# Optimization experiments

Measured on AMD Instinct MI355X. Metric: run time of the kernel, lower is better.

The kernel has to match this reference:

```python
import jax, jax.numpy as jnp
import numpy as np

B, TT, C, H, S, DF = 4, 2048, 2048, 32, 64, 7168
TC = 512            # chunk_len
NC = TT // TC       # number of chunks
N_LAYER, LAYER_ID = 12, 1
EPS = 1e-5
HS_DIV = float(np.sqrt(S))  # head_size_divisor


def layernorm(x, g, b):
    m = jnp.mean(x, axis=-1, keepdims=True)
    v = jnp.mean(jnp.square(x - m), axis=-1, keepdims=True)
    return (x - m) * jax.lax.rsqrt(v + EPS) * g + b


def time_shift(x):  # ZeroPad2d((0,0,1,-1)): x[t] <- x[t-1], x[0] <- 0
    return jnp.pad(x, ((0, 0), (1, 0), (0, 0)))[:, :-1, :]


def setup_inputs() -> dict:
    key = jax.random.key(0)
    ks = jax.random.split(key, 8)
    r10 = 1.0 - LAYER_ID / N_LAYER          # ratio_1_to_almost0
    r01 = LAYER_ID / (N_LAYER - 1)          # ratio_0_to_1
    ddd = np.arange(C, dtype=np.float64) / C
    f32 = lambda a: jnp.asarray(a, jnp.float32)
    hh = np.arange(H, dtype=np.float64)
    scale = 0.02
    W = lambda k, sh: (jax.random.normal(k, sh, jnp.float32) * scale)
    return {
        'x': jax.random.normal(ks[0], (B, TT, C), jnp.float32),
        'ln1_g': jnp.ones((C,), jnp.float32), 'ln1_b': jnp.zeros((C,), jnp.float32),
        'ln2_g': jnp.ones((C,), jnp.float32), 'ln2_b': jnp.zeros((C,), jnp.float32),
        'att_mix_k': f32(ddd ** r10),
        'att_mix_v': f32(ddd ** r10 + 0.3 * r01),
        'att_mix_r': f32(ddd ** (0.5 * r10)),
        'time_decay': f32(-8.0 + 7.0 * (hh / (H - 1)) ** (0.7 + 1.3 * r01)),
        'time_faaaa': jnp.full((H,), 0.05, jnp.float32),
        'Wr': W(ks[1], (C, C)), 'Wk': W(ks[2], (C, C)),
        'Wv': W(ks[3], (C, C)), 'Wo': W(ks[4], (C, C)),
        'lnx_g': jnp.ones((C,), jnp.float32), 'lnx_b': jnp.zeros((C,), jnp.float32),
        'ffn_mix_k': f32(ddd ** r10), 'ffn_mix_r': f32(ddd ** r10),
        'Wfk': W(ks[5], (C, DF)), 'Wfr': W(ks[6], (C, C)), 'Wfv': W(ks[7], (DF, C)),
    }


def _forward(x, ln1_g, ln1_b, ln2_g, ln2_b, att_mix_k, att_mix_v, att_mix_r,
             time_decay, time_faaaa, Wr, Wk, Wv, Wo, lnx_g, lnx_b,
             ffn_mix_k, ffn_mix_r, Wfk, Wfr, Wfv):
    # ---- RWKV5 TimeMix on ln1(x) ----
    h1 = layernorm(x, ln1_g, ln1_b)
    xx = time_shift(h1)
    xk = h1 * att_mix_k + xx * (1.0 - att_mix_k)
    xv = h1 * att_mix_v + xx * (1.0 - att_mix_v)
    xr = h1 * att_mix_r + xx * (1.0 - att_mix_r)
    r = (xr @ Wr).reshape(B, TT, H, S).transpose(0, 2, 1, 3)  # [B,H,TT,S]
    k = (xk @ Wk).reshape(B, TT, H, S).transpose(0, 2, 1, 3)
    v = (xv @ Wv).reshape(B, TT, H, S).transpose(0, 2, 1, 3)

    w = jnp.exp(-jnp.exp(time_decay))     # [H], per-head decay in (0,1)
    u = time_faaaa                         # [H], diagonal 'bonus'
    ws = w ** TC                           # chunk-level state decay
    t = jnp.arange(TC)
    wk = w[:, None] ** (TC - 1 - t)[None, :]   # [H,TC]: w^(T-1-t)
    wb = w[:, None] ** t[None, :]              # [H,TC]: w^t
    ii, jj = t[:, None], t[None, :]
    expo = jnp.where(jj < ii, ii - jj - 1, 0)
    # Wm[h,i,j] = w^(i-j-1) if j<i ; u if j==i ; 0 if j>i
    Wm = jnp.where(jj < ii, w[:, None, None] ** expo[None], 0.0)
    Wm = Wm + jnp.eye(TC, dtype=x.dtype)[None] * u[:, None, None]  # [H,TC,TC]

    rc = r.reshape(B, H, NC, TC, S).transpose(2, 0, 1, 3, 4)  # [NC,B,H,TC,S]
    kc = k.reshape(B, H, NC, TC, S).transpose(2, 0, 1, 3, 4)
    vc = v.reshape(B, H, NC, TC, S).transpose(2, 0, 1, 3, 4)

    def step(s, inp):  # s: [B,H,S,S] carried state
        rr, kk, vv = inp
        a = jnp.einsum('bhts,bhus->bhtu', rr, kk) * Wm[None]        # masked decay attn
        out = jnp.einsum('bhtu,bhus->bhts', a, vv)
        out = out + jnp.einsum('bhts,bhsu->bhtu', rr, s) * wb[None, :, :, None]
        s_new = ws[None, :, None, None] * s + jnp.einsum(
            'bhts,bhtu->bhsu', kk * wk[None, :, :, None], vv)
        return s_new, out

    s0 = jnp.zeros((B, H, S, S), x.dtype)
    _, xout = jax.lax.scan(step, s0, (rc, kc, vc))  # [NC,B,H,TC,S]
    xa = xout.transpose(1, 0, 3, 2, 4).reshape(B, TT, H, S)

    # GroupNorm(H groups over C) on x / sqrt(head_size)
    xa = xa / HS_DIV
    m = jnp.mean(xa, axis=-1, keepdims=True)
    va = jnp.mean(jnp.square(xa - m), axis=-1, keepdims=True)
    xa = (xa - m) * jax.lax.rsqrt(va + EPS)
    xa = xa * lnx_g.reshape(H, S) + lnx_b.reshape(H, S)
    x = x + xa.reshape(B, TT, C) @ Wo

    # ---- ChannelMix (gated squared-ReLU FFN) on ln2(x) ----
    h2 = layernorm(x, ln2_g, ln2_b)
    xx2 = time_shift(h2)
    xk2 = h2 * ffn_mix_k + xx2 * (1.0 - ffn_mix_k)
    xr2 = h2 * ffn_mix_r + xx2 * (1.0 - ffn_mix_r)
    kf = jnp.square(jax.nn.relu(xk2 @ Wfk))
    kv = kf @ Wfv
    return x + jax.nn.sigmoid(xr2 @ Wfr) * kv


def reference(x, ln1_g, ln1_b, ln2_g, ln2_b, att_mix_k, att_mix_v, att_mix_r,
              time_decay, time_faaaa, Wr, Wk, Wv, Wo, lnx_g, lnx_b,
              ffn_mix_k, ffn_mix_r, Wfk, Wfr, Wfv):
    return _forward(x, ln1_g, ln1_b, ln2_g, ln2_b, att_mix_k, att_mix_v,
                    att_mix_r, time_decay, time_faaaa, Wr, Wk, Wv, Wo,
                    lnx_g, lnx_b, ffn_mix_k, ffn_mix_r, Wfk, Wfr, Wfv)
```

## Files before the change

### kernel.cpp

```cpp
#include <hip/hip_runtime.h>

#define B_   4
#define TT_  2048
#define C_   2048
#define H_   32
#define S_   64
#define DF_  7168
#define TCH  512
#define NCH  4

typedef unsigned short u16;
typedef __bf16 bf16x8 __attribute__((ext_vector_type(8)));
typedef float  f32x4  __attribute__((ext_vector_type(4)));

__device__ __forceinline__ u16 f2bf(float f) {
  unsigned u = __builtin_bit_cast(unsigned, f);
  u = u + 0x7FFFu + ((u >> 16) & 1u);
  return (u16)(u >> 16);
}
__device__ __forceinline__ float bf2f(u16 v) {
  unsigned u = ((unsigned)v) << 16;
  return __builtin_bit_cast(float, u);
}

#define GLOAD16(g, l) __builtin_amdgcn_global_load_lds( \
    (const __attribute__((address_space(1))) void*)(g), \
    (__attribute__((address_space(3))) void*)(l), 16, 0, 0)

__device__ __forceinline__ void vmcnt6() { asm volatile("s_waitcnt vmcnt(6)" ::: "memory"); }
__device__ __forceinline__ void vmcnt0() { asm volatile("s_waitcnt vmcnt(0)" ::: "memory"); }

__global__ __launch_bounds__(256) void wcvt_t(const float* __restrict__ W,
                                              u16* __restrict__ Wt, int K, int Nfull,
                                              int n0off) {
  __shared__ alignas(16) float tile[32][33];
  int nloc = blockIdx.x * 32, k0 = blockIdx.y * 32;
  int tx = threadIdx.x & 31, ty = threadIdx.x >> 5;
  for (int r = ty; r < 32; r += 8)
    tile[r][tx] = W[(size_t)(k0 + r) * Nfull + n0off + nloc + tx];
  __syncthreads();
  for (int r = ty; r < 32; r += 8)
    Wt[(size_t)(nloc + r) * K + k0 + tx] = f2bf(tile[tx][r]);
}

__global__ __launch_bounds__(256) void ln_rows(const float* __restrict__ x,
                                               const float* __restrict__ g,
                                               const float* __restrict__ b,
                                               u16* __restrict__ out) {
  const int row = blockIdx.x;
  const float* xr = x + (size_t)row * C_;
  float v[8]; float s = 0.f, s2 = 0.f;
#pragma unroll
  for (int i = 0; i < 8; i++) { v[i] = xr[threadIdx.x + i * 256]; s += v[i]; s2 += v[i] * v[i]; }
#pragma unroll
  for (int o = 32; o > 0; o >>= 1) { s += __shfl_down(s, o); s2 += __shfl_down(s2, o); }
  __shared__ float rs[4], rs2[4];
  int wid = threadIdx.x >> 6, lane = threadIdx.x & 63;
  if (lane == 0) { rs[wid] = s; rs2[wid] = s2; }
  __syncthreads();
  s = rs[0] + rs[1] + rs[2] + rs[3];
  s2 = rs2[0] + rs2[1] + rs2[2] + rs2[3];
  float m = s * (1.f / C_);
  float var = s2 * (1.f / C_) - m * m;
  float inv = rsqrtf(var + 1e-5f);
  u16* orow = out + (size_t)row * C_;
#pragma unroll
  for (int i = 0; i < 8; i++) {
    int c = threadIdx.x + i * 256;
    orow[c] = f2bf((v[i] - m) * inv * g[c] + b[c]);
  }
}

__global__ void wtabs_k(const float* __restrict__ td, float* __restrict__ wb_tab,
                        float* __restrict__ wk_tab, float* __restrict__ wspow) {
  int h = blockIdx.x, t = threadIdx.x;
  float w = expf(-expf(td[h]));
  wb_tab[h * TCH + t] = powf(w, (float)t);
  wk_tab[h * TCH + t] = powf(w, (float)(TCH - 1 - t));
  if (t == 0) wspow[h] = powf(w, (float)TCH);
}

__device__ __forceinline__ void mix_body(const u16* cur, const u16* prev, bool hasp,
                                         const float* mc, u16* dst) {
  ushort4 c0 = *(const ushort4*)cur;
  ushort4 c1 = *(const ushort4*)(cur + 4);
  ushort4 p0 = {0, 0, 0, 0}, p1 = {0, 0, 0, 0};
  if (hasp) { p0 = *(const ushort4*)prev; p1 = *(const ushort4*)(prev + 4); }
  float4 mA = *(const float4*)mc;
  float4 mB = *(const float4*)(mc + 4);
  ushort4 r0, r1;
  r0.x = f2bf(bf2f(c0.x) * mA.x + bf2f(p0.x) * (1.f - mA.x));
  r0.y = f2bf(bf2f(c0.y) * mA.y + bf2f(p0.y) * (1.f - mA.y));
  r0.z = f2bf(bf2f(c0.z) * mA.z + bf2f(p0.z) * (1.f - mA.z));
  r0.w = f2bf(bf2f(c0.w) * mA.w + bf2f(p0.w) * (1.f - mA.w));
  r1.x = f2bf(bf2f(c1.x) * mB.x + bf2f(p1.x) * (1.f - mB.x));
  r1.y = f2bf(bf2f(c1.y) * mB.y + bf2f(p1.y) * (1.f - mB.y));
  r1.z = f2bf(bf2f(c1.z) * mB.z + bf2f(p1.z) * (1.f - mB.z));
  r1.w = f2bf(bf2f(c1.w) * mB.w + bf2f(p1.w) * (1.f - mB.w));
  *(ushort4*)dst = r0;
  *(ushort4*)(dst + 4) = r1;
}

__global__ __launch_bounds__(256) void mix3(const u16* __restrict__ h,
                                            const float* __restrict__ mk,
                                            const float* __restrict__ mv,
                                            const float* __restrict__ mr,
                                            u16* __restrict__ xk, u16* __restrict__ xv,
                                            u16* __restrict__ xr) {
  size_t i8 = (size_t)blockIdx.x * 256 + threadIdx.x;
  size_t off = i8 * 8;
  int c0 = (int)(off & (C_ - 1));
  int row = (int)(i8 >> 8);
  bool hasp = (row & (TT_ - 1)) != 0;
  const u16* cur = h + off;
  const u16* prev = cur - C_;
  mix_body(cur, prev, hasp, mk + c0, xk + off);
  mix_body(cur, prev, hasp, mv + c0, xv + off);
  mix_body(cur, prev, hasp, mr + c0, xr + off);
}

__global__ __launch_bounds__(256) void mix2(const u16* __restrict__ h,
                                            const float* __restrict__ mk,
                                            const float* __restrict__ mr,
                                            u16* __restrict__ xk, u16* __restrict__ xr) {
  size_t i8 = (size_t)blockIdx.x * 256 + threadIdx.x;
  size_t off = i8 * 8;
  int c0 = (int)(off & (C_ - 1));
  int row = (int)(i8 >> 8);
  bool hasp = (row & (TT_ - 1)) != 0;
  const u16* cur = h + off;
  const u16* prev = cur - C_;
  mix_body(cur, prev, hasp, mk + c0, xk + off);
  mix_body(cur, prev, hasp, mr + c0, xr + off);
}

template <int EPI>
__global__ __launch_bounds__(512) void gemm3(const u16* __restrict__ A,
                                             const u16* __restrict__ Bt,
                                             void* __restrict__ Cv,
                                             const float* __restrict__ res,
                                             const u16* __restrict__ srp,
                                             int N, int K, int lda, int ldb, int gy) {
  __shared__ alignas(16) char smem[3 * 49152];
  const int nwg = gridDim.x, qq = nwg >> 3;
  const int wg = (int)(blockIdx.x & 7) * qq + (int)(blockIdx.x >> 3);
  const int bx = wg / gy, by = wg % gy;
  const int tid = threadIdx.x, w = tid >> 6, lane = tid & 63;
  const int fr = lane & 15, fq = lane >> 4;
  const int m0 = bx * 128, n0 = by * 256;
  const int wm = (w >> 2) * 64, wn = (w & 3) * 64;
  const int rowS = tid >> 3;
  const int colS = ((tid & 7) * 8) ^ ((rowS & 7) << 3);
  const u16* Ag = A + (size_t)(m0 + rowS) * lda + colS;
  const u16* Bg = Bt + (size_t)(n0 + rowS) * ldb + colS;
  const int NT = K >> 6;

  f32x4 acc[4][4];
#pragma unroll
  for (int m = 0; m < 4; m++)
#pragma unroll
    for (int n = 0; n < 4; n++) acc[m][n] = (f32x4){0.f, 0.f, 0.f, 0.f};

#define STG_A(buf, k0, j) GLOAD16(Ag + (size_t)((j) * 64) * lda + (k0), \
    smem + (buf) * 49152 + (j) * 8192 + w * 1024)
#define STG_B(buf, k0, j) GLOAD16(Bg + (size_t)((j) * 64) * ldb + (k0), \
    smem + (buf) * 49152 + 16384 + (j) * 8192 + w * 1024)
#define RD_A(buf, kk, m) (*(const bf16x8*)(smem + (buf) * 49152 + \
    ((((wm + (m) * 16 + fr) * 128) + (kk) * 64 + fq * 16) ^ (((wm + (m) * 16 + fr) & 7) << 4))))
#define RD_B(buf, kk, n) (*(const bf16x8*)(smem + (buf) * 49152 + 16384 + \
    ((((wn + (n) * 16 + fr) * 128) + (kk) * 64 + fq * 16) ^ (((wn + (n) * 16 + fr) & 7) << 4))))

  STG_A(0, 0, 0); STG_A(0, 0, 1);
  STG_B(0, 0, 0); STG_B(0, 0, 1); STG_B(0, 0, 2); STG_B(0, 0, 3);
  STG_A(1, 64, 0); STG_A(1, 64, 1);
  STG_B(1, 64, 0); STG_B(1, 64, 1); STG_B(1, 64, 2); STG_B(1, 64, 3);
  vmcnt6();
  __builtin_amdgcn_s_barrier();

  int bufc = 0;
  for (int t = 0; t < NT; t++) {
    int b2 = bufc + 2; if (b2 >= 3) b2 -= 3;
    const bool st = (t + 2) < NT;
    const int k2 = (t + 2) << 6;
    bf16x8 av[4], bv[4];

#pragma unroll
    for (int m = 0; m < 4; m++) av[m] = RD_A(bufc, 0, m);
    bv[0] = RD_B(bufc, 0, 0); bv[1] = RD_B(bufc, 0, 1);
    if (st) STG_A(b2, k2, 0);
    __builtin_amdgcn_s_barrier();
    __builtin_amdgcn_s_setprio(1);
#pragma unroll
    for (int m = 0; m < 4; m++) {
      acc[m][0] = __builtin_amdgcn_mfma_f32_16x16x32_bf16(av[m], bv[0], acc[m][0], 0, 0, 0);
      acc[m][1] = __builtin_amdgcn_mfma_f32_16x16x32_bf16(av[m], bv[1], acc[m][1], 0, 0, 0);
    }
    __builtin_amdgcn_s_setprio(0);
    __builtin_amdgcn_s_barrier();

    bv[2] = RD_B(bufc, 0, 2); bv[3] = RD_B(bufc, 0, 3);
    if (st) { STG_A(b2, k2, 1); STG_B(b2, k2, 0); }
    __builtin_amdgcn_s_barrier();
    __builtin_amdgcn_s_setprio(1);
#pragma unroll
    for (int m = 0; m < 4; m++) {
      acc[m][2] = __builtin_amdgcn_mfma_f32_16x16x32_bf16(av[m], bv[2], acc[m][2], 0, 0, 0);
      acc[m][3] = __builtin_amdgcn_mfma_f32_16x16x32_bf16(av[m], bv[3], acc[m][3], 0, 0, 0);
    }
    __builtin_amdgcn_s_setprio(0);
    __builtin_amdgcn_s_barrier();

#pragma unroll
    for (int m = 0; m < 4; m++) av[m] = RD_A(bufc, 1, m);
    bv[0] = RD_B(bufc, 1, 0); bv[1] = RD_B(bufc, 1, 1);
    if (st) { STG_B(b2, k2, 1); STG_B(b2, k2, 2); }
    __builtin_amdgcn_s_barrier();
    __builtin_amdgcn_s_setprio(1);
#pragma unroll
    for (int m = 0; m < 4; m++) {
      acc[m][0] = __builtin_amdgcn_mfma_f32_16x16x32_bf16(av[m], bv[0], acc[m][0], 0, 0, 0);
      acc[m][1] = __builtin_amdgcn_mfma_f32_16x16x32_bf16(av[m], bv[1], acc[m][1], 0, 0, 0);
    }
    __builtin_amdgcn_s_setprio(0);
    __builtin_amdgcn_s_barrier();

    bv[2] = RD_B(bufc, 1, 2); bv[3] = RD_B(bufc, 1, 3);
    if (st) STG_B(b2, k2, 3);
    if (st) vmcnt6(); else vmcnt0();
    __builtin_amdgcn_s_barrier();
    __builtin_amdgcn_s_setprio(1);
#pragma unroll
    for (int m = 0; m < 4; m++) {
      acc[m][2] = __builtin_amdgcn_mfma_f32_16x16x32_bf16(av[m], bv[2], acc[m][2], 0, 0, 0);
      acc[m][3] = __builtin_amdgcn_mfma_f32_16x16x32_bf16(av[m], bv[3], acc[m][3], 0, 0, 0);
    }
    __builtin_amdgcn_s_setprio(0);
    __builtin_amdgcn_s_barrier();

    bufc = bufc + 1 == 3 ? 0 : bufc + 1;
  }
#undef STG_A
#undef STG_B
#undef RD_A
#undef RD_B

#pragma unroll
  for (int m = 0; m < 4; m++)
#pragma unroll
    for (int n = 0; n < 4; n++)
#pragma unroll
      for (int j = 0; j < 4; j++) {
        int row = m0 + wm + m * 16 + fq * 4 + j;
        int col = n0 + wn + n * 16 + fr;
        size_t idx = (size_t)row * N + col;
        float v = acc[m][n][j];
        if (EPI == 0) ((u16*)Cv)[idx] = f2bf(v);
        else if (EPI == 1) ((float*)Cv)[idx] = v + res[idx];
        else if (EPI == 2) { float r = v > 0.f ? v : 0.f; ((u16*)Cv)[idx] = f2bf(r * r); }
        else if (EPI == 3) ((u16*)Cv)[idx] = f2bf(1.f / (1.f + expf(-v)));
        else {
          float pvv = ((float*)Cv)[idx];
          ((float*)Cv)[idx] = pvv + bf2f(srp[idx]) * v;
        }
      }
}

__global__ __launch_bounds__(256) void kvsum_m(const u16* __restrict__ K,
                                               const u16* __restrict__ V,
                                               const float* __restrict__ wk_tab,
                                               float* __restrict__ SC) {
  const int bh = blockIdx.x & 127, c = blockIdx.x >> 7;
  const int b = bh >> 5, h = bh & 31;
  const int tid = threadIdx.x, w = tid >> 6, lane = tid & 63;
  const int fr = lane & 15, fq = lane >> 4;
  const size_t chunkbase = (size_t)b * TT_ + (size_t)c * TCH;
  const u16* Kp = K + chunkbase * C_ + h * 64;
  const u16* Vp = V + chunkbase * C_ + h * 64;
  __shared__ alignas(16) u16 Kts[64 * 128];
  __shared__ alignas(16) u16 Vts[64 * 128];
  f32x4 acc[4];
#pragma unroll
  for (int n = 0; n < 4; n++) acc[n] = (f32x4){0.f, 0.f, 0.f, 0.f};

  for (int tb = 0; tb < 4; tb++) {
    __syncthreads();
    const int u = tid >> 1;
    const int tg = tb * 128 + u;
    const float wkv = wk_tab[h * TCH + tg];
#pragma unroll
    for (int i = 0; i < 4; i++) {
      int s0 = (tid & 1) * 32 + i * 8;
      uint4 dK = *(const uint4*)(Kp + (size_t)tg * C_ + s0);
      uint4 dV = *(const uint4*)(Vp + (size_t)tg * C_ + s0);
      const u16* ek = (const u16*)&dK;
      const u16* ev = (const u16*)&dV;
#pragma unroll
      for (int j = 0; j < 8; j++) {
        int s = s0 + j;
        int byte = s * 256 + u * 2;
        byte ^= (s & 7) << 4;
        *(u16*)((char*)Kts + byte) = f2bf(bf2f(ek[j]) * wkv);
        *(u16*)((char*)Vts + byte) = ev[j];
      }
    }
    __syncthreads();
#pragma unroll
    for (int kk = 0; kk < 4; kk++) {
      int rbyteA = (w * 16 + fr) * 256 + kk * 64 + fq * 16;
      rbyteA ^= (fr & 7) << 4;
      bf16x8 av = *(const bf16x8*)((char*)Kts + rbyteA);
#pragma unroll
      for (int n = 0; n < 4; n++) {
        int rbyteB = (n * 16 + fr) * 256 + kk * 64 + fq * 16;
        rbyteB ^= (fr & 7) << 4;
        bf16x8 bv = *(const bf16x8*)((char*)Vts + rbyteB);
        acc[n] = __builtin_amdgcn_mfma_f32_16x16x32_bf16(av, bv, acc[n], 0, 0, 0);
      }
    }
  }
  float* out = SC + ((size_t)c * 128 + bh) * 4096;
#pragma unroll
  for (int n = 0; n < 4; n++)
#pragma unroll
    for (int j = 0; j < 4; j++) {
      int srow = w * 16 + fq * 4 + j;
      int scol = n * 16 + fr;
      out[srow * 64 + scol] = acc[n][j];
    }
}

__global__ __launch_bounds__(256) void stcomb(const float* __restrict__ SC,
                                              u16* __restrict__ STt,
                                              const float* __restrict__ wspow) {
  const int bh = blockIdx.x;
  const float ws = wspow[bh & 31];
  const int tid = threadIdx.x;
#pragma unroll
  for (int e = 0; e < 16; e++) {
    int idxT = e * 256 + tid;
    int s = idxT >> 6, sp = idxT & 63;
    int src = sp * 64 + s;
    float st = 0.f;
#pragma unroll
    for (int c = 0; c < 4; c++) {
      STt[((size_t)c * 128 + bh) * 4096 + idxT] = f2bf(st);
      st = ws * st + SC[((size_t)c * 128 + bh) * 4096 + src];
    }
  }
}

__global__ __launch_bounds__(256) void att_out_m(const u16* __restrict__ R,
                                                 const u16* __restrict__ K,
                                                 const u16* __restrict__ V,
                                                 const u16* __restrict__ STt,
                                                 const float* __restrict__ wb_tab,
                                                 const float* __restrict__ u_vec,
                                                 u16* __restrict__ xa) {
  const int bh = blockIdx.x;
  const int ti = blockIdx.y;
  const int c  = blockIdx.z;
  const int b = bh >> 5, h = bh & 31;
  const int tid = threadIdx.x, w = tid >> 6, lane = tid & 63;
  const int fr = lane & 15, fq = lane >> 4;
  const int t0 = ti * 64;
  const size_t chunkbase = (size_t)b * TT_ + (size_t)c * TCH;
  const u16* Rp = R + (chunkbase + t0) * C_ + h * 64;
  const u16* Kp = K + chunkbase * C_ + h * 64;
  const u16* Vp = V + chunkbase * C_ + h * 64;

  __shared__ alignas(16) u16 Rs[64 * 64];
  __shared__ alignas(16) u16 Ks[64 * 64];
  __shared__ alignas(16) u16 Vts[64 * 64];
  __shared__ alignas(16) u16 Xs[64 * 64];
  __shared__ float wbs[512];

#pragma unroll
  for (int it = 0; it < 2; it++) {
    int r = (tid >> 3) + it * 32;
    int cb = (tid & 7) * 16;
    uint4 d = *(const uint4*)((const char*)(Rp + (size_t)r * C_) + cb);
    int byte = (r * 128 + cb) ^ ((r & 7) << 4);
    *(uint4*)((char*)Rs + byte) = d;
  }
  const u16* stg = STt + ((size_t)c * 128 + bh) * 4096;
#pragma unroll
  for (int it = 0; it < 2; it++) {
    int s = (tid >> 3) + it * 32;
    int cb = (tid & 7) * 16;
    uint4 d = *(const uint4*)((const char*)(stg + (size_t)s * 64) + cb);
    int byte = (s * 128 + cb) ^ ((s & 7) << 4);
    *(uint4*)((char*)Xs + byte) = d;
  }
  wbs[tid] = wb_tab[h * TCH + tid];
  wbs[tid + 256] = wb_tab[h * TCH + tid + 256];
  const float uh = u_vec[h];
  __syncthreads();

  f32x4 pv[4];
#pragma unroll
  for (int n = 0; n < 4; n++) pv[n] = (f32x4){0.f, 0.f, 0.f, 0.f};
#pragma unroll
  for (int kk = 0; kk < 2; kk++) {
    int rbA = ((w * 16 + fr) * 128 + kk * 64 + fq * 16) ^ ((fr & 7) << 4);
    bf16x8 av = *(const bf16x8*)((char*)Rs + rbA);
#pragma unroll
    for (int n = 0; n < 4; n++) {
      int rbB = ((n * 16 + fr) * 128 + kk * 64 + fq * 16) ^ ((fr & 7) << 4);
      bf16x8 bv = *(const bf16x8*)((char*)Xs + rbB);
      pv[n] = __builtin_amdgcn_mfma_f32_16x16x32_bf16(av, bv, pv[n], 0, 0, 0);
    }
  }
#pragma unroll
  for (int n = 0; n < 4; n++)
#pragma unroll
    for (int j = 0; j < 4; j++) {
      int tg = t0 + w * 16 + fq * 4 + j;
      pv[n][j] *= wbs[tg];
    }

  for (int ub = 0; ub <= ti; ub++) {
    const int u0 = ub * 64;
    __syncthreads();
#pragma unroll
    for (int it = 0; it < 2; it++) {
      int r = (tid >> 3) + it * 32;
      int cb = (tid & 7) * 16;
      uint4 d = *(const uint4*)((const char*)(Kp + (size_t)(u0 + r) * C_) + cb);
      int byte = (r * 128 + cb) ^ ((r & 7) << 4);
      *(uint4*)((char*)Ks + byte) = d;
    }
#pragma unroll
    for (int it = 0; it < 2; it++) {
      int u = (tid >> 3) + it * 32;
      int s0 = (tid & 7) * 8;
      uint4 d = *(const uint4*)(Vp + (size_t)(u0 + u) * C_ + s0);
      const u16* ev = (const u16*)&d;
#pragma unroll
      for (int j = 0; j < 8; j++) {
        int s = s0 + j;
        int byte = (s * 128 + u * 2) ^ ((s & 7) << 4);
        *(u16*)((char*)Vts + byte) = ev[j];
      }
    }
    __syncthreads();
    f32x4 accA[4];
#pragma unroll
    for (int n = 0; n < 4; n++) accA[n] = (f32x4){0.f, 0.f, 0.f, 0.f};
#pragma unroll
    for (int kk = 0; kk < 2; kk++) {
      int rbA = ((w * 16 + fr) * 128 + kk * 64 + fq * 16) ^ ((fr & 7) << 4);
      bf16x8 av = *(const bf16x8*)((char*)Rs + rbA);
#pragma unroll
      for (int n = 0; n < 4; n++) {
        int rbB = ((n * 16 + fr) * 128 + kk * 64 + fq * 16) ^ ((fr & 7) << 4);
        bf16x8 bv = *(const bf16x8*)((char*)Ks + rbB);
        accA[n] = __builtin_amdgcn_mfma_f32_16x16x32_bf16(av, bv, accA[n], 0, 0, 0);
      }
    }
#pragma unroll
    for (int n = 0; n < 4; n++) {
#pragma unroll
      for (int j = 0; j < 4; j++) {
        int tl = w * 16 + fq * 4 + j;
        int tg = t0 + tl;
        int u = u0 + n * 16 + fr;
        int d = tg - u;
        float f = (d > 0) ? wbs[d - 1] : ((d == 0) ? uh : 0.f);
        int byte = (tl * 128 + (n * 16 + fr) * 2) ^ ((tl & 7) << 4);
        *(u16*)((char*)Xs + byte) = f2bf(accA[n][j] * f);
      }
    }
#pragma unroll
    for (int kk = 0; kk < 2; kk++) {
      int rbA = ((w * 16 + fr) * 128 + kk * 64 + fq * 16) ^ ((fr & 7) << 4);
      bf16x8 ap = *(const bf16x8*)((char*)Xs + rbA);
#pragma unroll
      for (int n = 0; n < 4; n++) {
        int rbB = ((n * 16 + fr) * 128 + kk * 64 + fq * 16) ^ ((fr & 7) << 4);
        bf16x8 vp = *(const bf16x8*)((char*)Vts + rbB);
        pv[n] = __builtin_amdgcn_mfma_f32_16x16x32_bf16(ap, vp, pv[n], 0, 0, 0);
      }
    }
  }
  u16* xout = xa + (chunkbase + t0) * C_ + h * 64;
#pragma unroll
  for (int n = 0; n < 4; n++)
#pragma unroll
    for (int j = 0; j < 4; j++) {
      int tl = w * 16 + fq * 4 + j;
      xout[(size_t)tl * C_ + n * 16 + fr] = f2bf(pv[n][j]);
    }
}

__global__ __launch_bounds__(256) void gnorm(const u16* __restrict__ xa,
                                             const float* __restrict__ g,
                                             const float* __restrict__ b,
                                             u16* __restrict__ out) {
  const int row = blockIdx.x;
  const int lane = threadIdx.x & 63, wv = threadIdx.x >> 6;
  const u16* xp = xa + (size_t)row * C_;
  u16* op = out + (size_t)row * C_;
  for (int h = wv; h < 32; h += 4) {
    float v = bf2f(xp[h * 64 + lane]) * 0.125f;
    float s = v, s2 = v * v;
#pragma unroll
    for (int o = 32; o > 0; o >>= 1) { s += __shfl_down(s, o); s2 += __shfl_down(s2, o); }
    s = __shfl(s, 0); s2 = __shfl(s2, 0);
    float m = s * (1.f / 64.f), var = s2 * (1.f / 64.f) - m * m;
    float nv = (v - m) * rsqrtf(var + 1e-5f);
    op[h * 64 + lane] = f2bf(nv * g[h * 64 + lane] + b[h * 64 + lane]);
  }
}

extern "C" void kernel_launch(void* const* d_in, const int* in_sizes, int n_in,
                              void* d_out, int out_size, void* d_ws, size_t ws_size,
                              hipStream_t stream) {
  (void)in_sizes; (void)n_in; (void)out_size; (void)ws_size;
  const float* x    = (const float*)d_in[0];
  const float* ln1g = (const float*)d_in[1];
  const float* ln1b = (const float*)d_in[2];
  const float* ln2g = (const float*)d_in[3];
  const float* ln2b = (const float*)d_in[4];
  const float* amk  = (const float*)d_in[5];
  const float* amv  = (const float*)d_in[6];
  const float* amr  = (const float*)d_in[7];
  const float* tdec = (const float*)d_in[8];
  const float* tfaa = (const float*)d_in[9];
  const float* Wr   = (const float*)d_in[10];
  const float* Wk   = (const float*)d_in[11];
  const float* Wv   = (const float*)d_in[12];
  const float* Wo   = (const float*)d_in[13];
  const float* lnxg = (const float*)d_in[14];
  const float* lnxb = (const float*)d_in[15];
  const float* fmk  = (const float*)d_in[16];
  const float* fmr  = (const float*)d_in[17];
  const float* Wfk  = (const float*)d_in[18];
  const float* Wfr  = (const float*)d_in[19];
  const float* Wfv  = (const float*)d_in[20];

  char* ws = (char*)d_ws;
  const size_t MB = 1ull << 20;
  u16* WR  = (u16*)(ws + 0 * MB);
  u16* WK  = (u16*)(ws + 8 * MB);
  u16* WV  = (u16*)(ws + 16 * MB);
  u16* WO  = (u16*)(ws + 24 * MB);
  u16* WFR = (u16*)(ws + 32 * MB);
  u16* WFK = (u16*)(ws + 40 * MB);
  u16* WFV = (u16*)(ws + 68 * MB);
  u16* H1  = (u16*)(ws + 96 * MB);
  u16* XR  = (u16*)(ws + 128 * MB);
  u16* XK  = (u16*)(ws + 160 * MB);
  u16* XV  = (u16*)(ws + 192 * MB);
  float* WBT = (float*)(ws + 224 * MB);
  float* WKT = (float*)(ws + 224 * MB + 65536);
  float* WSP = (float*)(ws + 224 * MB + 131072);
  float* SCb = (float*)(ws + 0 * MB);
  u16* STTb  = (u16*)(ws + 8 * MB);
  u16* RB   = H1;
  u16* KB   = XR;
  u16* VB   = XK;
  u16* XA   = XV;
  u16* XAN  = H1;
  u16* H2   = XV;
  u16* XK2  = WR;
  u16* XR2  = H1;
  u16* SR   = XR;
  u16* KFH  = XK;
  float* OUT = (float*)d_out;

  dim3 blk(256), gblk(512);
  wcvt_t<<<dim3(64, 64), blk, 0, stream>>>(Wr, WR, 2048, 2048, 0);
  wcvt_t<<<dim3(64, 64), blk, 0, stream>>>(Wk, WK, 2048, 2048, 0);
  wcvt_t<<<dim3(64, 64), blk, 0, stream>>>(Wv, WV, 2048, 2048, 0);
  wcvt_t<<<dim3(64, 64), blk, 0, stream>>>(Wo, WO, 2048, 2048, 0);
  wcvt_t<<<dim3(64, 64), blk, 0, stream>>>(Wfr, WFR, 2048, 2048, 0);
  wcvt_t<<<dim3(224, 64), blk, 0, stream>>>(Wfk, WFK, 2048, 7168, 0);
  wcvt_t<<<dim3(64, 224), blk, 0, stream>>>(Wfv, WFV, 7168, 2048, 0);

  ln_rows<<<8192, blk, 0, stream>>>(x, ln1g, ln1b, H1);
  mix3<<<8192, blk, 0, stream>>>(H1, amk, amv, amr, XK, XV, XR);
  gemm3<0><<<512, gblk, 0, stream>>>(XR, WR, RB, nullptr, nullptr, 2048, 2048, 2048, 2048, 8);
  gemm3<0><<<512, gblk, 0, stream>>>(XK, WK, KB, nullptr, nullptr, 2048, 2048, 2048, 2048, 8);
  gemm3<0><<<512, gblk, 0, stream>>>(XV, WV, VB, nullptr, nullptr, 2048, 2048, 2048, 2048, 8);

  wtabs_k<<<32, 512, 0, stream>>>(tdec, WBT, WKT, WSP);
  kvsum_m<<<512, blk, 0, stream>>>(KB, VB, WKT, SCb);
  stcomb<<<128, blk, 0, stream>>>(SCb, STTb, WSP);
  att_out_m<<<dim3(128, 8, 4), blk, 0, stream>>>(RB, KB, VB, STTb, WBT, tfaa, XA);

  gnorm<<<8192, blk, 0, stream>>>(XA, lnxg, lnxb, XAN);
  gemm3<1><<<512, gblk, 0, stream>>>(XAN, WO, OUT, x, nullptr, 2048, 2048, 2048, 2048, 8);

  ln_rows<<<8192, blk, 0, stream>>>(OUT, ln2g, ln2b, H2);
  mix2<<<8192, blk, 0, stream>>>(H2, fmk, fmr, XK2, XR2);
  gemm3<3><<<512, gblk, 0, stream>>>(XR2, WFR, SR, nullptr, nullptr, 2048, 2048, 2048, 2048, 8);

  for (int half = 0; half < 2; half++) {
    const u16* a_half = XK2 + (size_t)half * 4096 * 2048;
    gemm3<2><<<896, gblk, 0, stream>>>(a_half, WFK, KFH, nullptr, nullptr,
                                       7168, 2048, 2048, 2048, 28);
    gemm3<9><<<256, gblk, 0, stream>>>(KFH, WFV, OUT + (size_t)half * 4096 * 2048,
                                       nullptr, SR + (size_t)half * 4096 * 2048,
                                       2048, 7168, 7168, 7168, 8);
  }
}
```

Baseline: 1.347 ms.

## Add 256x256-tile double-buffered GEMM kernel with staged loads for most projections

Adds a new gemm4 kernel that uses 256x256 output tiles, two LDS buffers, and global-to-LDS loads spread across four MFMA phases per k-step, fenced by barriers and s_setprio. The R/K/V, output, FFN-receptance and FFN-key GEMMs now use it with half as many workgroups, while the down projection stays on gemm3, whose epilogue is cut to just the accumulate path and plain bf16 store. The larger tile gives more reuse per byte loaded and overlaps loads with math, but it halves the grid to 256 blocks, which may leave compute units idle. It also raises register and LDS pressure.

```diff
diff --git a/kernel.cpp b/kernel.cpp
--- a/kernel.cpp
+++ b/kernel.cpp
@@ -28,6 +28,7 @@
     (__attribute__((address_space(3))) void*)(l), 16, 0, 0)
 
 __device__ __forceinline__ void vmcnt6() { asm volatile("s_waitcnt vmcnt(6)" ::: "memory"); }
+__device__ __forceinline__ void vmcnt2() { asm volatile("s_waitcnt vmcnt(2)" ::: "memory"); }
 __device__ __forceinline__ void vmcnt0() { asm volatile("s_waitcnt vmcnt(0)" ::: "memory"); }
 
 __global__ __launch_bounds__(256) void wcvt_t(const float* __restrict__ W,
@@ -132,6 +133,132 @@
   const u16* prev = cur - C_;
   mix_body(cur, prev, hasp, mk + c0, xk + off);
   mix_body(cur, prev, hasp, mr + c0, xr + off);
+}
+
+template <int EPI>
+__global__ __launch_bounds__(512) void gemm4(const u16* __restrict__ A,
+                                             const u16* __restrict__ Bt,
+                                             void* __restrict__ Cv,
+                                             const float* __restrict__ res,
+                                             int N, int K, int lda, int ldb, int gy) {
+  __shared__ alignas(16) u16 As[2][256 * 64];
+  __shared__ alignas(16) u16 Bs[2][256 * 64];
+  const int nwg = gridDim.x, qq = nwg >> 3;
+  const int wg = (int)(blockIdx.x & 7) * qq + (int)(blockIdx.x >> 3);
+  const int bx = wg / gy, by = wg % gy;
+  const int tid = threadIdx.x, w = tid >> 6, lane = tid & 63;
+  const int fr = lane & 15, fq = lane >> 4;
+  const int m0 = bx * 256, n0 = by * 256;
+  const int wm = (w >> 2) * 128;
+  const int wn = (w & 3) * 64;
+  const int rowS = tid >> 3;
+  const int colS = ((tid & 7) * 8) ^ ((rowS & 7) << 3);
+  const u16* Ag = A + (size_t)(m0 + rowS) * lda + colS;
+  const u16* Bg = Bt + (size_t)(n0 + rowS) * ldb + colS;
+  const int NT = K >> 6;
+
+  f32x4 acc[8][4];
+#pragma unroll
+  for (int m = 0; m < 8; m++)
+#pragma unroll
+    for (int n = 0; n < 4; n++) acc[m][n] = (f32x4){0.f, 0.f, 0.f, 0.f};
+
+#define STG_A4(p, k0, j) GLOAD16(Ag + (size_t)((j) * 64) * lda + (k0), \
+    (char*)As[p] + (j) * 8192 + w * 1024)
+#define STG_B4(p, k0, j) GLOAD16(Bg + (size_t)((j) * 64) * ldb + (k0), \
+    (char*)Bs[p] + (j) * 8192 + w * 1024)
+#define RD_A4(p, kk, r) (*(const bf16x8*)((char*)As[p] + \
+    ((((r) * 128) + (kk) * 64 + fq * 16) ^ (((r) & 7) << 4))))
+#define RD_B4(p, kk, r) (*(const bf16x8*)((char*)Bs[p] + \
+    ((((r) * 128) + (kk) * 64 + fq * 16) ^ (((r) & 7) << 4))))
+
+  STG_B4(0, 0, 0); STG_B4(0, 0, 1); STG_B4(0, 0, 2); STG_B4(0, 0, 3);
+  STG_A4(0, 0, 0); STG_A4(0, 0, 2); STG_A4(0, 0, 1); STG_A4(0, 0, 3);
+  vmcnt2();
+  __builtin_amdgcn_s_barrier();
+
+  for (int t = 0; t < NT; t++) {
+    const int p = t & 1;
+    const bool st = (t + 1) < NT;
+    const int k1 = (t + 1) << 6;
+    bf16x8 av[4], bv[4];
+
+#pragma unroll
+    for (int i = 0; i < 4; i++) av[i] = RD_A4(p, 0, wm + i * 16 + fr);
+#pragma unroll
+    for (int n = 0; n < 4; n++) bv[n] = RD_B4(p, 0, wn + n * 16 + fr);
+    if (st) { STG_B4(p ^ 1, k1, 0); STG_B4(p ^ 1, k1, 1); vmcnt2(); } else vmcnt0();
+    __builtin_amdgcn_s_barrier();
+    __builtin_amdgcn_s_setprio(1);
+#pragma unroll
+    for (int i = 0; i < 4; i++)
+#pragma unroll
+      for (int n = 0; n < 4; n++)
+        acc[i][n] = __builtin_amdgcn_mfma_f32_16x16x32_bf16(av[i], bv[n], acc[i][n], 0, 0, 0);
+    __builtin_amdgcn_s_setprio(0);
+    __builtin_amdgcn_s_barrier();
+
+#pragma unroll
+    for (int i = 0; i < 4; i++) av[i] = RD_A4(p, 0, wm + 64 + i * 16 + fr);
+    if (st) { STG_B4(p ^ 1, k1, 2); STG_B4(p ^ 1, k1, 3); vmcnt2(); }
+    __builtin_amdgcn_s_barrier();
+    __builtin_amdgcn_s_setprio(1);
+#pragma unroll
+    for (int i = 0; i < 4; i++)
+#pragma unroll
+      for (int n = 0; n < 4; n++)
+        acc[4 + i][n] = __builtin_amdgcn_mfma_f32_16x16x32_bf16(av[i], bv[n], acc[4 + i][n], 0, 0, 0);
+    __builtin_amdgcn_s_setprio(0);
+    __builtin_amdgcn_s_barrier();
+
+#pragma unroll
+    for (int i = 0; i < 4; i++) av[i] = RD_A4(p, 1, wm + i * 16 + fr);
+#pragma unroll
+    for (int n = 0; n < 4; n++) bv[n] = RD_B4(p, 1, wn + n * 16 + fr);
+    if (st) { STG_A4(p ^ 1, k1, 0); STG_A4(p ^ 1, k1, 2); vmcnt2(); }
+    __builtin_amdgcn_s_barrier();
+    __builtin_amdgcn_s_setprio(1);
+#pragma unroll
+    for (int i = 0; i < 4; i++)
+#pragma unroll
+      for (int n = 0; n < 4; n++)
+        acc[i][n] = __builtin_amdgcn_mfma_f32_16x16x32_bf16(av[i], bv[n], acc[i][n], 0, 0, 0);
+    __builtin_amdgcn_s_setprio(0);
+    __builtin_amdgcn_s_barrier();
+
+#pragma unroll
+    for (int i = 0; i < 4; i++) av[i] = RD_A4(p, 1, wm + 64 + i * 16 + fr);
+    if (st) { STG_A4(p ^ 1, k1, 1); STG_A4(p ^ 1, k1, 3); vmcnt2(); }
+    __builtin_amdgcn_s_barrier();
+    __builtin_amdgcn_s_setprio(1);
+#pragma unroll
+    for (int i = 0; i < 4; i++)
+#pragma unroll
+      for (int n = 0; n < 4; n++)
+        acc[4 + i][n] = __builtin_amdgcn_mfma_f32_16x16x32_bf16(av[i], bv[n], acc[4 + i][n], 0, 0, 0);
+    __builtin_amdgcn_s_setprio(0);
+    __builtin_amdgcn_s_barrier();
+  }
+#undef STG_A4
+#undef STG_B4
+#undef RD_A4
+#undef RD_B4
+
+#pragma unroll
+  for (int m = 0; m < 8; m++)
+#pragma unroll
+    for (int n = 0; n < 4; n++)
+#pragma unroll
+      for (int j = 0; j < 4; j++) {
+        int row = m0 + wm + m * 16 + fq * 4 + j;
+        int col = n0 + wn + n * 16 + fr;
+        size_t idx = (size_t)row * N + col;
+        float v = acc[m][n][j];
+        if (EPI == 0) ((u16*)Cv)[idx] = f2bf(v);
+        else if (EPI == 1) ((float*)Cv)[idx] = v + res[idx];
+        else if (EPI == 2) { float r = v > 0.f ? v : 0.f; ((u16*)Cv)[idx] = f2bf(r * r); }
+        else ((u16*)Cv)[idx] = f2bf(1.f / (1.f + expf(-v)));
+      }
 }
 
 template <int EPI>
@@ -254,14 +381,13 @@
         int col = n0 + wn + n * 16 + fr;
         size_t idx = (size_t)row * N + col;
         float v = acc[m][n][j];
-        if (EPI == 0) ((u16*)Cv)[idx] = f2bf(v);
-        else if (EPI == 1) ((float*)Cv)[idx] = v + res[idx];
-        else if (EPI == 2) { float r = v > 0.f ? v : 0.f; ((u16*)Cv)[idx] = f2bf(r * r); }
-        else if (EPI == 3) ((u16*)Cv)[idx] = f2bf(1.f / (1.f + expf(-v)));
-        else {
+        if (EPI == 9) {
           float pvv = ((float*)Cv)[idx];
           ((float*)Cv)[idx] = pvv + bf2f(srp[idx]) * v;
+        } else {
+          ((u16*)Cv)[idx] = f2bf(v);
         }
+        (void)res;
       }
 }
 
@@ -579,9 +705,9 @@
 
   ln_rows<<<8192, blk, 0, stream>>>(x, ln1g, ln1b, H1);
   mix3<<<8192, blk, 0, stream>>>(H1, amk, amv, amr, XK, XV, XR);
-  gemm3<0><<<512, gblk, 0, stream>>>(XR, WR, RB, nullptr, nullptr, 2048, 2048, 2048, 2048, 8);
-  gemm3<0><<<512, gblk, 0, stream>>>(XK, WK, KB, nullptr, nullptr, 2048, 2048, 2048, 2048, 8);
-  gemm3<0><<<512, gblk, 0, stream>>>(XV, WV, VB, nullptr, nullptr, 2048, 2048, 2048, 2048, 8);
+  gemm4<0><<<256, gblk, 0, stream>>>(XR, WR, RB, nullptr, 2048, 2048, 2048, 2048, 8);
+  gemm4<0><<<256, gblk, 0, stream>>>(XK, WK, KB, nullptr, 2048, 2048, 2048, 2048, 8);
+  gemm4<0><<<256, gblk, 0, stream>>>(XV, WV, VB, nullptr, 2048, 2048, 2048, 2048, 8);
 
   wtabs_k<<<32, 512, 0, stream>>>(tdec, WBT, WKT, WSP);
   kvsum_m<<<512, blk, 0, stream>>>(KB, VB, WKT, SCb);
@@ -589,15 +715,15 @@
   att_out_m<<<dim3(128, 8, 4), blk, 0, stream>>>(RB, KB, VB, STTb, WBT, tfaa, XA);
 
   gnorm<<<8192, blk, 0, stream>>>(XA, lnxg, lnxb, XAN);
-  gemm3<1><<<512, gblk, 0, stream>>>(XAN, WO, OUT, x, nullptr, 2048, 2048, 2048, 2048, 8);
+  gemm4<1><<<256, gblk, 0, stream>>>(XAN, WO, OUT, x, 2048, 2048, 2048, 2048, 8);
 
   ln_rows<<<8192, blk, 0, stream>>>(OUT, ln2g, ln2b, H2);
   mix2<<<8192, blk, 0, stream>>>(H2, fmk, fmr, XK2, XR2);
-  gemm3<3><<<512, gblk, 0, stream>>>(XR2, WFR, SR, nullptr, nullptr, 2048, 2048, 2048, 2048, 8);
+  gemm4<3><<<256, gblk, 0, stream>>>(XR2, WFR, SR, nullptr, 2048, 2048, 2048, 2048, 8);
 
   for (int half = 0; half < 2; half++) {
     const u16* a_half = XK2 + (size_t)half * 4096 * 2048;
-    gemm3<2><<<896, gblk, 0, stream>>>(a_half, WFK, KFH, nullptr, nullptr,
+    gemm4<2><<<448, gblk, 0, stream>>>(a_half, WFK, KFH, nullptr,
                                        7168, 2048, 2048, 2048, 28);
     gemm3<9><<<256, gblk, 0, stream>>>(KFH, WFV, OUT + (size_t)half * 4096 * 2048,
                                        nullptr, SR + (size_t)half * 4096 * 2048,
```

Result: faster. 1.261 ms (-6.4%).

## Enlarge GEMM tile to 256x256 with double buffering and split FFN along hidden dim

Applied to the files above, without the earlier changes.

The GEMM kernel moves from a 128x256 tile with triple-buffered LDS to a 256x256 tile with double-buffered A/B in LDS. Each wave now holds 8x4 accumulators, which doubles A reuse per loaded B and halves the grid. The FFN is also split along the hidden dimension DF instead of along rows, so the second GEMM accumulates two K-halves into OUT. This raises register and LDS pressure (128KB of LDS, about 128 accumulator VGPRs), lowers occupancy, and drops from three buffers to two, which shortens the prefetch distance.

```diff
diff --git a/kernel.cpp b/kernel.cpp
--- a/kernel.cpp
+++ b/kernel.cpp
@@ -27,7 +27,7 @@
     (const __attribute__((address_space(1))) void*)(g), \
     (__attribute__((address_space(3))) void*)(l), 16, 0, 0)
 
-__device__ __forceinline__ void vmcnt6() { asm volatile("s_waitcnt vmcnt(6)" ::: "memory"); }
+__device__ __forceinline__ void vmcnt2() { asm volatile("s_waitcnt vmcnt(2)" ::: "memory"); }
 __device__ __forceinline__ void vmcnt0() { asm volatile("s_waitcnt vmcnt(0)" ::: "memory"); }
 
 __global__ __launch_bounds__(256) void wcvt_t(const float* __restrict__ W,
@@ -135,117 +135,117 @@
 }
 
 template <int EPI>
-__global__ __launch_bounds__(512) void gemm3(const u16* __restrict__ A,
+__global__ __launch_bounds__(512) void gemm4(const u16* __restrict__ A,
                                              const u16* __restrict__ Bt,
                                              void* __restrict__ Cv,
                                              const float* __restrict__ res,
                                              const u16* __restrict__ srp,
                                              int N, int K, int lda, int ldb, int gy) {
-  __shared__ alignas(16) char smem[3 * 49152];
+  __shared__ alignas(16) u16 As[2][256 * 64];
+  __shared__ alignas(16) u16 Bs[2][256 * 64];
   const int nwg = gridDim.x, qq = nwg >> 3;
   const int wg = (int)(blockIdx.x & 7) * qq + (int)(blockIdx.x >> 3);
   const int bx = wg / gy, by = wg % gy;
   const int tid = threadIdx.x, w = tid >> 6, lane = tid & 63;
   const int fr = lane & 15, fq = lane >> 4;
-  const int m0 = bx * 128, n0 = by * 256;
-  const int wm = (w >> 2) * 64, wn = (w & 3) * 64;
+  const int m0 = bx * 256, n0 = by * 256;
+  const int wm = (w >> 2) * 128;
+  const int wn = (w & 3) * 64;
   const int rowS = tid >> 3;
   const int colS = ((tid & 7) * 8) ^ ((rowS & 7) << 3);
   const u16* Ag = A + (size_t)(m0 + rowS) * lda + colS;
   const u16* Bg = Bt + (size_t)(n0 + rowS) * ldb + colS;
   const int NT = K >> 6;
 
-  f32x4 acc[4][4];
-#pragma unroll
-  for (int m = 0; m < 4; m++)
+  f32x4 acc[8][4];
+#pragma unroll
+  for (int m = 0; m < 8; m++)
 #pragma unroll
     for (int n = 0; n < 4; n++) acc[m][n] = (f32x4){0.f, 0.f, 0.f, 0.f};
 
-#define STG_A(buf, k0, j) GLOAD16(Ag + (size_t)((j) * 64) * lda + (k0), \
-    smem + (buf) * 49152 + (j) * 8192 + w * 1024)
-#define STG_B(buf, k0, j) GLOAD16(Bg + (size_t)((j) * 64) * ldb + (k0), \
-    smem + (buf) * 49152 + 16384 + (j) * 8192 + w * 1024)
-#define RD_A(buf, kk, m) (*(const bf16x8*)(smem + (buf) * 49152 + \
-    ((((wm + (m) * 16 + fr) * 128) + (kk) * 64 + fq * 16) ^ (((wm + (m) * 16 + fr) & 7) << 4))))
-#define RD_B(buf, kk, n) (*(const bf16x8*)(smem + (buf) * 49152 + 16384 + \
-    ((((wn + (n) * 16 + fr) * 128) + (kk) * 64 + fq * 16) ^ (((wn + (n) * 16 + fr) & 7) << 4))))
-
-  STG_A(0, 0, 0); STG_A(0, 0, 1);
-  STG_B(0, 0, 0); STG_B(0, 0, 1); STG_B(0, 0, 2); STG_B(0, 0, 3);
-  STG_A(1, 64, 0); STG_A(1, 64, 1);
-  STG_B(1, 64, 0); STG_B(1, 64, 1); STG_B(1, 64, 2); STG_B(1, 64, 3);
-  vmcnt6();
+#define STG_A4(p, k0, j) GLOAD16(Ag + (size_t)((j) * 64) * lda + (k0), \
+    (char*)As[p] + (j) * 8192 + w * 1024)
+#define STG_B4(p, k0, j) GLOAD16(Bg + (size_t)((j) * 64) * ldb + (k0), \
+    (char*)Bs[p] + (j) * 8192 + w * 1024)
+#define RD_A4(p, kk, r) (*(const bf16x8*)((char*)As[p] + \
+    ((((r) * 128) + (kk) * 64 + fq * 16) ^ (((r) & 7) << 4))))
+#define RD_B4(p, kk, r) (*(const bf16x8*)((char*)Bs[p] + \
+    ((((r) * 128) + (kk) * 64 + fq * 16) ^ (((r) & 7) << 4))))
+
+  STG_B4(0, 0, 0); STG_B4(0, 0, 1); STG_B4(0, 0, 2); STG_B4(0, 0, 3);
+  STG_A4(0, 0, 0); STG_A4(0, 0, 2); STG_A4(0, 0, 1); STG_A4(0, 0, 3);
+  vmcnt2();
   __builtin_amdgcn_s_barrier();
 
-  int bufc = 0;
   for (int t = 0; t < NT; t++) {
-    int b2 = bufc + 2; if (b2 >= 3) b2 -= 3;
-    const bool st = (t + 2) < NT;
-    const int k2 = (t + 2) << 6;
+    const int p = t & 1;
+    const bool st = (t + 1) < NT;
+    const int k1 = (t + 1) << 6;
     bf16x8 av[4], bv[4];
 
 #pragma unroll
-    for (int m = 0; m < 4; m++) av[m] = RD_A(bufc, 0, m);
-    bv[0] = RD_B(bufc, 0, 0); bv[1] = RD_B(bufc, 0, 1);
-    if (st) STG_A(b2, k2, 0);
+    for (int i = 0; i < 4; i++) av[i] = RD_A4(p, 0, wm + i * 16 + fr);
+#pragma unroll
+    for (int n = 0; n < 4; n++) bv[n] = RD_B4(p, 0, wn + n * 16 + fr);
+    if (st) { STG_B4(p ^ 1, k1, 0); STG_B4(p ^ 1, k1, 1); vmcnt2(); } else vmcnt0();
     __builtin_amdgcn_s_barrier();
     __builtin_amdgcn_s_setprio(1);
 #pragma unroll
-    for (int m = 0; m < 4; m++) {
-      acc[m][0] = __builtin_amdgcn_mfma_f32_16x16x32_bf16(av[m], bv[0], acc[m][0], 0, 0, 0);
-      acc[m][1] = __builtin_amdgcn_mfma_f32_16x16x32_bf16(av[m], bv[1], acc[m][1], 0, 0, 0);
-    }
+    for (int i = 0; i < 4; i++)
+#pragma unroll
+      for (int n = 0; n < 4; n++)
+        acc[i][n] = __builtin_amdgcn_mfma_f32_16x16x32_bf16(av[i], bv[n], acc[i][n], 0, 0, 0);
     __builtin_amdgcn_s_setprio(0);
     __builtin_amdgcn_s_barrier();
 
-    bv[2] = RD_B(bufc, 0, 2); bv[3] = RD_B(bufc, 0, 3);
-    if (st) { STG_A(b2, k2, 1); STG_B(b2, k2, 0); }
+#pragma unroll
+    for (int i = 0; i < 4; i++) av[i] = RD_A4(p, 0, wm + 64 + i * 16 + fr);
+    if (st) { STG_B4(p ^ 1, k1, 2); STG_B4(p ^ 1, k1, 3); vmcnt2(); }
     __builtin_amdgcn_s_barrier();
     __builtin_amdgcn_s_setprio(1);
 #pragma unroll
-    for (int m = 0; m < 4; m++) {
-      acc[m][2] = __builtin_amdgcn_mfma_f32_16x16x32_bf16(av[m], bv[2], acc[m][2], 0, 0, 0);
-      acc[m][3] = __builtin_amdgcn_mfma_f32_16x16x32_bf16(av[m], bv[3], acc[m][3], 0, 0, 0);
-    }
+    for (int i = 0; i < 4; i++)
+#pragma unroll
+      for (int n = 0; n < 4; n++)
+        acc[4 + i][n] = __builtin_amdgcn_mfma_f32_16x16x32_bf16(av[i], bv[n], acc[4 + i][n], 0, 0, 0);
     __builtin_amdgcn_s_setprio(0);
     __builtin_amdgcn_s_barrier();
 
 #pragma unroll
-    for (int m = 0; m < 4; m++) av[m] = RD_A(bufc, 1, m);
-    bv[0] = RD_B(bufc, 1, 0); bv[1] = RD_B(bufc, 1, 1);
-    if (st) { STG_B(b2, k2, 1); STG_B(b2, k2, 2); }
+    for (int i = 0; i < 4; i++) av[i] = RD_A4(p, 1, wm + i * 16 + fr);
+#pragma unroll
+    for (int n = 0; n < 4; n++) bv[n] = RD_B4(p, 1, wn + n * 16 + fr);
+    if (st) { STG_A4(p ^ 1, k1, 0); STG_A4(p ^ 1, k1, 2); vmcnt2(); }
     __builtin_amdgcn_s_barrier();
     __builtin_amdgcn_s_setprio(1);
 #pragma unroll
-    for (int m = 0; m < 4; m++) {
-      acc[m][0] = __builtin_amdgcn_mfma_f32_16x16x32_bf16(av[m], bv[0], acc[m][0], 0, 0, 0);
-      acc[m][1] = __builtin_amdgcn_mfma_f32_16x16x32_bf16(av[m], bv[1], acc[m][1], 0, 0, 0);
-    }
+    for (int i = 0; i < 4; i++)
+#pragma unroll
+      for (int n = 0; n < 4; n++)
+        acc[i][n] = __builtin_amdgcn_mfma_f32_16x16x32_bf16(av[i], bv[n], acc[i][n], 0, 0, 0);
     __builtin_amdgcn_s_setprio(0);
     __builtin_amdgcn_s_barrier();
 
-    bv[2] = RD_B(bufc, 1, 2); bv[3] = RD_B(bufc, 1, 3);
-    if (st) STG_B(b2, k2, 3);
-    if (st) vmcnt6(); else vmcnt0();
+#pragma unroll
+    for (int i = 0; i < 4; i++) av[i] = RD_A4(p, 1, wm + 64 + i * 16 + fr);
+    if (st) { STG_A4(p ^ 1, k1, 1); STG_A4(p ^ 1, k1, 3); vmcnt2(); }
     __builtin_amdgcn_s_barrier();
     __builtin_amdgcn_s_setprio(1);
 #pragma unroll
-    for (int m = 0; m < 4; m++) {
-      acc[m][2] = __builtin_amdgcn_mfma_f32_16x16x32_bf16(av[m], bv[2], acc[m][2], 0, 0, 0);
-      acc[m][3] = __builtin_amdgcn_mfma_f32_16x16x32_bf16(av[m], bv[3], acc[m][3], 0, 0, 0);
-    }
+    for (int i = 0; i < 4; i++)
+#pragma unroll
+      for (int n = 0; n < 4; n++)
+        acc[4 + i][n] = __builtin_amdgcn_mfma_f32_16x16x32_bf16(av[i], bv[n], acc[4 + i][n], 0, 0, 0);
     __builtin_amdgcn_s_setprio(0);
     __builtin_amdgcn_s_barrier();
-
-    bufc = bufc + 1 == 3 ? 0 : bufc + 1;
-  }
-#undef STG_A
-#undef STG_B
-#undef RD_A
-#undef RD_B
-
-#pragma unroll
-  for (int m = 0; m < 4; m++)
+  }
+#undef STG_A4
+#undef STG_B4
+#undef RD_A4
+#undef RD_B4
+
+#pragma unroll
+  for (int m = 0; m < 8; m++)
 #pragma unroll
     for (int n = 0; n < 4; n++)
 #pragma unroll
@@ -579,9 +579,9 @@
 
   ln_rows<<<8192, blk, 0, stream>>>(x, ln1g, ln1b, H1);
   mix3<<<8192, blk, 0, stream>>>(H1, amk, amv, amr, XK, XV, XR);
-  gemm3<0><<<512, gblk, 0, stream>>>(XR, WR, RB, nullptr, nullptr, 2048, 2048, 2048, 2048, 8);
-  gemm3<0><<<512, gblk, 0, stream>>>(XK, WK, KB, nullptr, nullptr, 2048, 2048, 2048, 2048, 8);
-  gemm3<0><<<512, gblk, 0, stream>>>(XV, WV, VB, nullptr, nullptr, 2048, 2048, 2048, 2048, 8);
+  gemm4<0><<<256, gblk, 0, stream>>>(XR, WR, RB, nullptr, nullptr, 2048, 2048, 2048, 2048, 8);
+  gemm4<0><<<256, gblk, 0, stream>>>(XK, WK, KB, nullptr, nullptr, 2048, 2048, 2048, 2048, 8);
+  gemm4<0><<<256, gblk, 0, stream>>>(XV, WV, VB, nullptr, nullptr, 2048, 2048, 2048, 2048, 8);
 
   wtabs_k<<<32, 512, 0, stream>>>(tdec, WBT, WKT, WSP);
   kvsum_m<<<512, blk, 0, stream>>>(KB, VB, WKT, SCb);
@@ -589,18 +589,18 @@
   att_out_m<<<dim3(128, 8, 4), blk, 0, stream>>>(RB, KB, VB, STTb, WBT, tfaa, XA);
 
   gnorm<<<8192, blk, 0, stream>>>(XA, lnxg, lnxb, XAN);
-  gemm3<1><<<512, gblk, 0, stream>>>(XAN, WO, OUT, x, nullptr, 2048, 2048, 2048, 2048, 8);
+  gemm4<1><<<256, gblk, 0, stream>>>(XAN, WO, OUT, x, nullptr, 2048, 2048, 2048, 2048, 8);
 
   ln_rows<<<8192, blk, 0, stream>>>(OUT, ln2g, ln2b, H2);
   mix2<<<8192, blk, 0, stream>>>(H2, fmk, fmr, XK2, XR2);
-  gemm3<3><<<512, gblk, 0, stream>>>(XR2, WFR, SR, nullptr, nullptr, 2048, 2048, 2048, 2048, 8);
+  gemm4<3><<<256, gblk, 0, stream>>>(XR2, WFR, SR, nullptr, nullptr, 2048, 2048, 2048, 2048, 8);
 
   for (int half = 0; half < 2; half++) {
-    const u16* a_half = XK2 + (size_t)half * 4096 * 2048;
-    gemm3<2><<<896, gblk, 0, stream>>>(a_half, WFK, KFH, nullptr, nullptr,
-                                       7168, 2048, 2048, 2048, 28);
-    gemm3<9><<<256, gblk, 0, stream>>>(KFH, WFV, OUT + (size_t)half * 4096 * 2048,
-                                       nullptr, SR + (size_t)half * 4096 * 2048,
-                                       2048, 7168, 7168, 7168, 8);
-  }
-}
+    const u16* wfk_h = WFK + (size_t)half * 3584 * 2048;
+    gemm4<2><<<448, gblk, 0, stream>>>(XK2, wfk_h, KFH, nullptr, nullptr,
+                                       3584, 2048, 2048, 2048, 14);
+    const u16* wfv_h = WFV + (size_t)half * 3584;
+    gemm4<9><<<256, gblk, 0, stream>>>(KFH, wfv_h, OUT, nullptr, SR,
+                                       2048, 3584, 3584, 7168, 8);
+  }
+}
```

Result: faster. 1.311 ms, median of 2 (-2.7%).
